# Kernel optimization log

Hardware: AMD Instinct MI355X
Metric: run time of the kernel (lower is better)

## Reference

```python
import jax, jax.numpy as jnp
import numpy as np

BINS = 10

def setup_inputs() -> dict:
    key = jax.random.key(0)
    k1, k2, k3 = jax.random.split(key, 3)
    shape = (8, 128, 128, 180)  # (batch, h, w, num_anchors*num_classes)
    class_labels = jax.random.randint(k1, shape, 0, 2, dtype=jnp.int32)
    class_logits = jax.random.normal(k2, shape, dtype=jnp.float32)
    label_weights = jax.random.uniform(k3, shape, dtype=jnp.float32)
    return {"class_labels": class_labels, "class_logits": class_logits,
            "label_weights": label_weights}


def reference(class_labels, class_logits, label_weights):
    bins = BINS
    probs = jax.nn.sigmoid(class_logits)
    labels_f = class_labels.astype(class_logits.dtype)
    # gradient magnitude proxy: |p - label|
    p_norm = jnp.where(class_labels == 1, 1.0 - probs, probs)
    total_num = jnp.maximum(jnp.sum(label_weights), 1.0)
    valid = (label_weights > 0).astype(class_logits.dtype)
    # bin edges are i/bins with last edge = 1 + 1e-6; sigmoid output is in (0,1)
    # so floor(p*bins) clipped to [0, bins-1] reproduces the bin assignment
    bin_idx = jnp.clip(jnp.floor(p_norm * bins).astype(jnp.int32), 0, bins - 1)
    counts = jax.ops.segment_sum(valid.ravel(), bin_idx.ravel(), num_segments=bins)
    n = jnp.sum(counts > 0).astype(class_logits.dtype)
    per_bin_w = jnp.where(counts > 0, total_num / jnp.maximum(counts, 1.0), 0.0)
    beta = per_bin_w[bin_idx] * valid
    beta = jnp.where(n > 0, beta / jnp.maximum(n, 1.0), beta)
    # tf.nn.sigmoid_cross_entropy_with_logits
    x = class_logits
    bce = jnp.maximum(x, 0.0) - x * labels_f + jnp.log1p(jnp.exp(-jnp.abs(x)))
    return jnp.sum(bce * beta) / total_num
```

## Files before the change

kernel.cpp:

```cpp
#include <hip/hip_runtime.h>
#include <math.h>

#define BINS 10
#define K1_THREADS 256
#define K1_MAXBLOCKS 2048

__device__ const float TH[10] = {
    0.0f,
    -2.19722458f,
    -1.38629436f,
    -0.84729786f,
    -0.40546511f,
     0.0f,
     0.40546511f,
     0.84729786f,
     1.38629436f,
     2.19722458f
};

__device__ __forceinline__ void ghm_elem(int y, float x, float w,
                                         float* __restrict__ G,
                                         unsigned* __restrict__ C) {
    float xs = __int_as_float(__float_as_int(x) ^ (y << 31));
    bool  v  = (w > 0.0f);
    xs = v ? xs : -1e30f;
    C[0] += v;
    float e   = __expf(-fabsf(xs));
    float d   = 1.0f + e;
    float bce = fmaxf(xs, 0.0f) + __logf(d);
    G[0] += bce;
    #pragma unroll
    for (int b = 1; b < BINS; ++b) {
        bool ge = (xs >= TH[b]);
        C[b] += ge;
        G[b] += ge ? bce : 0.0f;
    }
}

__global__ __launch_bounds__(K1_THREADS, 8) void ghm_partial(
    const int*   __restrict__ labels,
    const float* __restrict__ logits,
    const float* __restrict__ weights,
    float*       __restrict__ partial,
    int nbatch, int n, int nb)
{
    const int tid  = blockIdx.x * K1_THREADS + threadIdx.x;
    const int T    = gridDim.x * K1_THREADS;

    float    G[BINS];
    unsigned C[BINS];
    #pragma unroll
    for (int b = 0; b < BINS; ++b) { G[b] = 0.0f; C[b] = 0u; }

    const int4*   lab4 = (const int4*)labels;
    const float4* log4 = (const float4*)logits;
    const float4* w4   = (const float4*)weights;

    int i = tid;
    if (nbatch > 0) {
        int4   a0 = lab4[i];
        float4 x0 = log4[i];
        float4 v0 = w4[i];
        #pragma unroll 2
        for (int bt = 1; bt < nbatch; ++bt) {
            const int i1 = i + T;
            int4   a1 = lab4[i1];
            float4 x1 = log4[i1];
            float4 v1 = w4[i1];
            ghm_elem(a0.x, x0.x, v0.x, G, C);
            ghm_elem(a0.y, x0.y, v0.y, G, C);
            ghm_elem(a0.z, x0.z, v0.z, G, C);
            ghm_elem(a0.w, x0.w, v0.w, G, C);
            a0 = a1; x0 = x1; v0 = v1; i = i1;
        }
        ghm_elem(a0.x, x0.x, v0.x, G, C);
        ghm_elem(a0.y, x0.y, v0.y, G, C);
        ghm_elem(a0.z, x0.z, v0.z, G, C);
        ghm_elem(a0.w, x0.w, v0.w, G, C);
    }

    for (int e = nbatch * T * 4 + tid; e < n; e += T)
        ghm_elem(labels[e], logits[e], weights[e], G, C);

    float g[BINS], c[BINS];
    #pragma unroll
    for (int b = 0; b < BINS; ++b) { g[b] = G[b]; c[b] = (float)C[b]; }
    #pragma unroll
    for (int off = 32; off > 0; off >>= 1) {
        #pragma unroll
        for (int b = 0; b < BINS; ++b) {
            c[b] += __shfl_down(c[b], off);
            g[b] += __shfl_down(g[b], off);
        }
    }
    __shared__ float redc[K1_THREADS / 64][BINS];
    __shared__ float redg[K1_THREADS / 64][BINS];
    const int wave = threadIdx.x >> 6, lane = threadIdx.x & 63;
    if (lane == 0) {
        #pragma unroll
        for (int b = 0; b < BINS; ++b) { redc[wave][b] = c[b]; redg[wave][b] = g[b]; }
    }
    __syncthreads();
    if (threadIdx.x < BINS) {
        float cc = 0.0f, gg = 0.0f;
        #pragma unroll
        for (int wv = 0; wv < K1_THREADS / 64; ++wv) {
            cc += redc[wv][threadIdx.x];
            gg += redg[wv][threadIdx.x];
        }
        partial[threadIdx.x * nb + blockIdx.x]          = cc;
        partial[(BINS + threadIdx.x) * nb + blockIdx.x] = gg;
    }
}

__global__ __launch_bounds__(1024) void ghm_final(
    const float* __restrict__ partial, float* __restrict__ out, int nb)
{
    const int tid = threadIdx.x;
    float acc[2 * BINS];
    #pragma unroll
    for (int b = 0; b < 2 * BINS; ++b) acc[b] = 0.0f;
    for (int j = tid; j < nb; j += 1024) {
        #pragma unroll
        for (int b = 0; b < 2 * BINS; ++b)
            acc[b] += partial[b * nb + j];
    }

    #pragma unroll
    for (int off = 32; off > 0; off >>= 1) {
        #pragma unroll
        for (int b = 0; b < 2 * BINS; ++b)
            acc[b] += __shfl_down(acc[b], off);
    }

    __shared__ float red[16][2 * BINS];
    const int wave = tid >> 6, lane = tid & 63;
    if (lane == 0) {
        #pragma unroll
        for (int b = 0; b < 2 * BINS; ++b) red[wave][b] = acc[b];
    }
    __syncthreads();

    if (tid == 0) {
        float cum_c[BINS], cum_g[BINS];
        #pragma unroll
        for (int b = 0; b < BINS; ++b) { cum_c[b] = 0.0f; cum_g[b] = 0.0f; }
        for (int wv = 0; wv < 16; ++wv) {
            #pragma unroll
            for (int b = 0; b < BINS; ++b) {
                cum_c[b] += red[wv][b];
                cum_g[b] += red[wv][BINS + b];
            }
        }
        float nn = 0.0f, res = 0.0f;
        #pragma unroll
        for (int b = 0; b < BINS; ++b) {
            float Cb = (b < BINS - 1) ? (cum_c[b] - cum_c[b + 1]) : cum_c[b];
            float Sb = (b < BINS - 1) ? (cum_g[b] - cum_g[b + 1]) : cum_g[b];
            if (Cb > 0.5f) {
                nn  += 1.0f;
                res += Sb / Cb;
            }
        }
        if (nn > 0.0f) res /= nn;
        out[0] = res;
    }
}

extern "C" void kernel_launch(void* const* d_in, const int* in_sizes, int n_in,
                              void* d_out, int out_size, void* d_ws, size_t ws_size,
                              hipStream_t stream) {
    const int*   labels  = (const int*)d_in[0];
    const float* logits  = (const float*)d_in[1];
    const float* weights = (const float*)d_in[2];
    float* out     = (float*)d_out;
    float* partial = (float*)d_ws;

    const int n = in_sizes[0];

    int nb = (int)(ws_size / (2 * BINS * sizeof(float)));
    if (nb > K1_MAXBLOCKS) nb = K1_MAXBLOCKS;
    if (nb < 1) nb = 1;

    const int T      = nb * K1_THREADS;
    const int nbatch = n / (4 * T);

    ghm_partial<<<nb, K1_THREADS, 0, stream>>>(labels, logits, weights, partial,
                                               nbatch, n, nb);
    ghm_final<<<1, 1024, 0, stream>>>(partial, out, nb);
}
```

Before: 89.48 us.

## Stream inputs via async global-to-LDS loads with per-wave multi-slot pipeline

The main loop is rebuilt so each wave owns a contiguous chunk and prefetches three tiles ahead using global_load_lds into per-wave LDS ring slots, gated by explicit vmcnt waits. Counters become float to avoid int-to-float conversion, the grid size is fixed at 1440 blocks, and the threshold table moves into a compile-time constant. The aim is more bytes in flight to hide memory latency in a bandwidth-bound reduction. The cost is 48KB of LDS per block, which may limit occupancy, and the hand-written vmcnt counts depend on the exact instruction sequence the compiler emits.

```diff
diff --git a/kernel.cpp b/kernel.cpp
--- a/kernel.cpp
+++ b/kernel.cpp
@@ -3,113 +3,124 @@
 
 #define BINS 10
 #define K1_THREADS 256
-#define K1_MAXBLOCKS 2048
-
-__device__ const float TH[10] = {
-    0.0f,
-    -2.19722458f,
-    -1.38629436f,
-    -0.84729786f,
-    -0.40546511f,
-     0.0f,
-     0.40546511f,
-     0.84729786f,
-     1.38629436f,
-     2.19722458f
-};
+#define WPB   4
+#define DEPTH 3
+#define NSLOT 4
+#define TILE  256
+#define SLOT_BYTES 3072
 
 __device__ __forceinline__ void ghm_elem(int y, float x, float w,
                                          float* __restrict__ G,
-                                         unsigned* __restrict__ C) {
+                                         float* __restrict__ C) {
+    constexpr float TH[10] = {
+        0.0f, -2.19722458f, -1.38629436f, -0.84729786f, -0.40546511f,
+        0.0f,  0.40546511f,  0.84729786f,  1.38629436f,  2.19722458f };
     float xs = __int_as_float(__float_as_int(x) ^ (y << 31));
     bool  v  = (w > 0.0f);
     xs = v ? xs : -1e30f;
-    C[0] += v;
+    C[0] += v ? 1.0f : 0.0f;
     float e   = __expf(-fabsf(xs));
-    float d   = 1.0f + e;
-    float bce = fmaxf(xs, 0.0f) + __logf(d);
+    float bce = fmaxf(xs, 0.0f) + __logf(1.0f + e);
     G[0] += bce;
     #pragma unroll
     for (int b = 1; b < BINS; ++b) {
         bool ge = (xs >= TH[b]);
-        C[b] += ge;
+        C[b] += ge ? 1.0f : 0.0f;
         G[b] += ge ? bce : 0.0f;
     }
 }
 
-__global__ __launch_bounds__(K1_THREADS, 8) void ghm_partial(
+#define GLD_LDS16(gsrc, ldst)                                                  \
+    __builtin_amdgcn_global_load_lds(                                          \
+        (const __attribute__((address_space(1))) void*)(gsrc),                 \
+        (__attribute__((address_space(3))) void*)(ldst), 16, 0, 0)
+
+__global__ __launch_bounds__(K1_THREADS) void ghm_partial(
     const int*   __restrict__ labels,
     const float* __restrict__ logits,
     const float* __restrict__ weights,
     float*       __restrict__ partial,
-    int nbatch, int n, int nb)
+    int NT, int n, int nb, int covered)
 {
-    const int tid  = blockIdx.x * K1_THREADS + threadIdx.x;
-    const int T    = gridDim.x * K1_THREADS;
+    __shared__ __align__(16) char ldsbuf[WPB][NSLOT][SLOT_BYTES];
+    __shared__ float redc[WPB][BINS], redg[WPB][BINS];
 
-    float    G[BINS];
-    unsigned C[BINS];
+    const int tid  = threadIdx.x;
+    const int wid  = tid >> 6;
+    const int lane = tid & 63;
+    const int wgl  = blockIdx.x * WPB + wid;
+    const int base0 = wgl * NT * TILE;
+
+    float G[BINS], C[BINS];
     #pragma unroll
-    for (int b = 0; b < BINS; ++b) { G[b] = 0.0f; C[b] = 0u; }
+    for (int b = 0; b < BINS; ++b) { G[b] = 0.0f; C[b] = 0.0f; }
 
-    const int4*   lab4 = (const int4*)labels;
-    const float4* log4 = (const float4*)logits;
-    const float4* w4   = (const float4*)weights;
+    const int*   labp = labels  + base0;
+    const float* logp = logits  + base0;
+    const float* wtp  = weights + base0;
 
-    int i = tid;
-    if (nbatch > 0) {
-        int4   a0 = lab4[i];
-        float4 x0 = log4[i];
-        float4 v0 = w4[i];
-        #pragma unroll 2
-        for (int bt = 1; bt < nbatch; ++bt) {
-            const int i1 = i + T;
-            int4   a1 = lab4[i1];
-            float4 x1 = log4[i1];
-            float4 v1 = w4[i1];
-            ghm_elem(a0.x, x0.x, v0.x, G, C);
-            ghm_elem(a0.y, x0.y, v0.y, G, C);
-            ghm_elem(a0.z, x0.z, v0.z, G, C);
-            ghm_elem(a0.w, x0.w, v0.w, G, C);
-            a0 = a1; x0 = x1; v0 = v1; i = i1;
+    auto stage = [&](int k) {
+        char* slot = &ldsbuf[wid][k & (NSLOT - 1)][0];
+        const int off = k * TILE + lane * 4;
+        GLD_LDS16(labp + off, slot);
+        GLD_LDS16(logp + off, slot + 1024);
+        GLD_LDS16(wtp  + off, slot + 2048);
+    };
+    auto consume = [&](int k) {
+        const char* slot = &ldsbuf[wid][k & (NSLOT - 1)][0];
+        int4   lb = *(const int4*)  (slot +        lane * 16);
+        float4 xv = *(const float4*)(slot + 1024 + lane * 16);
+        float4 wv = *(const float4*)(slot + 2048 + lane * 16);
+        ghm_elem(lb.x, xv.x, wv.x, G, C);
+        ghm_elem(lb.y, xv.y, wv.y, G, C);
+        ghm_elem(lb.z, xv.z, wv.z, G, C);
+        ghm_elem(lb.w, xv.w, wv.w, G, C);
+    };
+
+    if (NT > DEPTH) {
+        stage(0); stage(1); stage(2);
+        for (int t = 0; t < NT - DEPTH; ++t) {
+            stage(t + DEPTH);
+            asm volatile("s_waitcnt vmcnt(9)" ::: "memory");
+            consume(t);
         }
-        ghm_elem(a0.x, x0.x, v0.x, G, C);
-        ghm_elem(a0.y, x0.y, v0.y, G, C);
-        ghm_elem(a0.z, x0.z, v0.z, G, C);
-        ghm_elem(a0.w, x0.w, v0.w, G, C);
+        asm volatile("s_waitcnt vmcnt(6)" ::: "memory");
+        consume(NT - 3);
+        asm volatile("s_waitcnt vmcnt(3)" ::: "memory");
+        consume(NT - 2);
+        asm volatile("s_waitcnt vmcnt(0)" ::: "memory");
+        consume(NT - 1);
+    } else {
+        for (int t = 0; t < NT; ++t) {
+            stage(t);
+            asm volatile("s_waitcnt vmcnt(0)" ::: "memory");
+            consume(t);
+        }
     }
 
-    for (int e = nbatch * T * 4 + tid; e < n; e += T)
-        ghm_elem(labels[e], logits[e], weights[e], G, C);
+    const int T = nb * K1_THREADS;
+    for (int e2 = covered + blockIdx.x * K1_THREADS + tid; e2 < n; e2 += T)
+        ghm_elem(labels[e2], logits[e2], weights[e2], G, C);
 
-    float g[BINS], c[BINS];
-    #pragma unroll
-    for (int b = 0; b < BINS; ++b) { g[b] = G[b]; c[b] = (float)C[b]; }
     #pragma unroll
     for (int off = 32; off > 0; off >>= 1) {
         #pragma unroll
         for (int b = 0; b < BINS; ++b) {
-            c[b] += __shfl_down(c[b], off);
-            g[b] += __shfl_down(g[b], off);
+            C[b] += __shfl_down(C[b], off);
+            G[b] += __shfl_down(G[b], off);
         }
     }
-    __shared__ float redc[K1_THREADS / 64][BINS];
-    __shared__ float redg[K1_THREADS / 64][BINS];
-    const int wave = threadIdx.x >> 6, lane = threadIdx.x & 63;
     if (lane == 0) {
         #pragma unroll
-        for (int b = 0; b < BINS; ++b) { redc[wave][b] = c[b]; redg[wave][b] = g[b]; }
+        for (int b = 0; b < BINS; ++b) { redc[wid][b] = C[b]; redg[wid][b] = G[b]; }
     }
     __syncthreads();
-    if (threadIdx.x < BINS) {
+    if (tid < BINS) {
         float cc = 0.0f, gg = 0.0f;
         #pragma unroll
-        for (int wv = 0; wv < K1_THREADS / 64; ++wv) {
-            cc += redc[wv][threadIdx.x];
-            gg += redg[wv][threadIdx.x];
-        }
-        partial[threadIdx.x * nb + blockIdx.x]          = cc;
-        partial[(BINS + threadIdx.x) * nb + blockIdx.x] = gg;
+        for (int wv = 0; wv < WPB; ++wv) { cc += redc[wv][tid]; gg += redg[wv][tid]; }
+        partial[tid * nb + blockIdx.x]          = cc;
+        partial[(BINS + tid) * nb + blockIdx.x] = gg;
     }
 }
 
@@ -125,14 +136,12 @@
         for (int b = 0; b < 2 * BINS; ++b)
             acc[b] += partial[b * nb + j];
     }
-
     #pragma unroll
     for (int off = 32; off > 0; off >>= 1) {
         #pragma unroll
         for (int b = 0; b < 2 * BINS; ++b)
             acc[b] += __shfl_down(acc[b], off);
     }
-
     __shared__ float red[16][2 * BINS];
     const int wave = tid >> 6, lane = tid & 63;
     if (lane == 0) {
@@ -140,7 +149,6 @@
         for (int b = 0; b < 2 * BINS; ++b) red[wave][b] = acc[b];
     }
     __syncthreads();
-
     if (tid == 0) {
         float cum_c[BINS], cum_g[BINS];
         #pragma unroll
@@ -157,10 +165,7 @@
         for (int b = 0; b < BINS; ++b) {
             float Cb = (b < BINS - 1) ? (cum_c[b] - cum_c[b + 1]) : cum_c[b];
             float Sb = (b < BINS - 1) ? (cum_g[b] - cum_g[b + 1]) : cum_g[b];
-            if (Cb > 0.5f) {
-                nn  += 1.0f;
-                res += Sb / Cb;
-            }
+            if (Cb > 0.5f) { nn += 1.0f; res += Sb / Cb; }
         }
         if (nn > 0.0f) res /= nn;
         out[0] = res;
@@ -178,14 +183,15 @@
 
     const int n = in_sizes[0];
 
-    int nb = (int)(ws_size / (2 * BINS * sizeof(float)));
-    if (nb > K1_MAXBLOCKS) nb = K1_MAXBLOCKS;
-    if (nb < 1) nb = 1;
+    int nb = 1440;
+    const size_t row_bytes = 2 * BINS * sizeof(float);
+    if (ws_size < row_bytes * 1440) nb = 720;
+    if (ws_size < row_bytes * 720)  nb = 360;
 
-    const int T      = nb * K1_THREADS;
-    const int nbatch = n / (4 * T);
+    const int NT      = n / (nb * WPB * TILE);
+    const int covered = NT * nb * WPB * TILE;
 
     ghm_partial<<<nb, K1_THREADS, 0, stream>>>(labels, logits, weights, partial,
-                                               nbatch, n, nb);
+                                               NT, n, nb, covered);
     ghm_final<<<1, 1024, 0, stream>>>(partial, out, nb);
 }
```

After: 83.84 us. 1.07x faster.
